# Kernel tuning notes

Measured on AMD Instinct MI355X. Metric: run time of the kernel, lower is better.

Reference implementation:

```python
import jax, jax.numpy as jnp
import numpy as np

EMBED, HEADS, LEVELS, POINTS, CAMS, ZANCH = 256, 8, 4, 8, 6, 4
HEAD_DIM = EMBED // HEADS
NQ, BS = 10000, 1
SHAPES = np.array([[92, 160], [46, 80], [23, 40], [12, 20]], dtype=np.int64)
NV = int((SHAPES[:, 0] * SHAPES[:, 1]).sum())  # 19560


def setup_inputs() -> dict:
    key = jax.random.key(0)
    ks = jax.random.split(key, 10)
    f = lambda k, s, sc=1.0: jax.random.normal(k, s, dtype=jnp.float32) * sc
    lsi = np.concatenate([[0], np.cumsum(SHAPES[:, 0] * SHAPES[:, 1])[:-1]]).astype(np.int64)
    return dict(
        query=f(ks[0], (BS, NQ, EMBED)),
        query_pos=f(ks[1], (BS, NQ, EMBED)),
        value=f(ks[2], (CAMS, NV, BS, EMBED)),
        reference_points=jax.random.uniform(ks[3], (CAMS, BS, NQ, ZANCH, 2), dtype=jnp.float32),
        bev_mask=jax.random.bernoulli(ks[4], 0.3, (CAMS, BS, NQ, ZANCH)),
        spatial_shapes=jnp.asarray(SHAPES),
        level_start_index=jnp.asarray(lsi),
        Wv=f(ks[5], (EMBED, EMBED), 0.02), bv=jnp.zeros((EMBED,), jnp.float32),
        Woff=f(ks[6], (EMBED, HEADS * LEVELS * POINTS * 2), 0.02),
        boff=f(ks[7], (HEADS * LEVELS * POINTS * 2,), 0.5),
        Watt=f(ks[8], (EMBED, HEADS * LEVELS * POINTS), 0.02),
        batt=jnp.zeros((HEADS * LEVELS * POINTS,), jnp.float32),
        Wout=f(ks[9], (EMBED, EMBED), 0.02), bout=jnp.zeros((EMBED,), jnp.float32),
    )


def _bilinear_gather(v2, x, y, H, W):
    # v2: (BH, H*W, hd); x, y: (BH, N) pixel coords. grid_sample bilinear,
    # align_corners=False, padding_mode='zeros' semantics.
    x0 = jnp.floor(x); y0 = jnp.floor(y)
    lx = x - x0; ly = y - y0
    x0i = x0.astype(jnp.int32); y0i = y0.astype(jnp.int32)
    out = jnp.zeros(x.shape + (v2.shape[-1],), v2.dtype)
    for dx, dy, w in ((0, 0, (1 - lx) * (1 - ly)), (1, 0, lx * (1 - ly)),
                      (0, 1, (1 - lx) * ly), (1, 1, lx * ly)):
        xi = x0i + dx; yi = y0i + dy
        valid = (xi >= 0) & (xi < W) & (yi >= 0) & (yi < H)
        idx = jnp.clip(yi, 0, H - 1) * W + jnp.clip(xi, 0, W - 1)
        g = jnp.take_along_axis(v2, idx[..., None], axis=1)
        out = out + g * (w * valid.astype(v2.dtype))[..., None]
    return out


def _ms_deform_attn(q, v, ref, shapes, lsi, Wv, bv, Woff, boff, Watt, batt):
    # q: (B, nq, C); v: (B, nv, C); ref: (B, nq, D, 2)
    B, nq, C = q.shape
    v = (v @ Wv + bv).reshape(B, -1, HEADS, HEAD_DIM)
    off = (q @ Woff + boff).reshape(B, nq, HEADS, LEVELS, POINTS, 2)
    attw = jax.nn.softmax((q @ Watt + batt).reshape(B, nq, HEADS, LEVELS * POINTS), axis=-1)
    attw = attw.reshape(B, nq, HEADS, LEVELS, POINTS)
    # offset normalizer: (w_l, h_l) per level
    norm = jnp.asarray(np.stack([shapes[:, 1], shapes[:, 0]], -1), q.dtype)  # (L, 2)
    off = off / norm[None, None, None, :, None, :]
    off = off.reshape(B, nq, HEADS, LEVELS, POINTS // ZANCH, ZANCH, 2)
    loc = (ref[:, :, None, None, None] + off).reshape(B, nq, HEADS, LEVELS, POINTS, 2)
    acc = jnp.zeros((B, HEADS, nq, HEAD_DIM), q.dtype)
    for l in range(LEVELS):
        H, W = int(shapes[l, 0]), int(shapes[l, 1])
        s = int(lsi[l])
        vl = v[:, s:s + H * W].transpose(0, 2, 1, 3).reshape(B * HEADS, H * W, HEAD_DIM)
        ll = loc[:, :, :, l].transpose(0, 2, 1, 3, 4).reshape(B * HEADS, nq * POINTS, 2)
        x = ll[..., 0] * W - 0.5
        y = ll[..., 1] * H - 0.5
        samp = _bilinear_gather(vl, x, y, H, W).reshape(B, HEADS, nq, POINTS, HEAD_DIM)
        w = attw[:, :, :, l].transpose(0, 2, 1, 3)  # (B, HEADS, nq, POINTS)
        acc = acc + (samp * w[..., None]).sum(3)
    return acc.transpose(0, 2, 1, 3).reshape(B, nq, C)


def reference(query, query_pos, value, reference_points, bev_mask, spatial_shapes,
              level_start_index, Wv, bv, Woff, boff, Watt, batt, Wout, bout):
    shapes = np.asarray(spatial_shapes)
    lsi = np.asarray(level_start_index)
    B, nq, C = query.shape
    cams = value.shape[0]
    q = query + query_pos
    # replicate queries per camera (equivalent to rebatch-by-mask: unselected
    # outputs are masked out before accumulation)
    q_cam = jnp.broadcast_to(q[:, None], (B, cams, nq, C)).reshape(B * cams, nq, C)
    v = value.transpose(2, 0, 1, 3).reshape(B * cams, -1, C)
    ref = reference_points.transpose(1, 0, 2, 3, 4).reshape(B * cams, nq, ZANCH, 2)
    out = _ms_deform_attn(q_cam, v, ref, shapes, lsi, Wv, bv, Woff, boff, Watt, batt)
    out = out.reshape(B, cams, nq, C)
    # query selection per camera uses batch 0 of bev_mask, as in the original
    m = (bev_mask[:, 0].sum(-1) > 0)  # (cams, nq)
    slots = (out * m[None, :, :, None].astype(out.dtype)).sum(1)  # (B, nq, C)
    count = (bev_mask.sum(-1) > 0).astype(query.dtype).transpose(1, 2, 0).sum(-1)
    count = jnp.maximum(count, 1.0)  # (B, nq)
    slots = slots / count[..., None]
    # dropout in eval mode is identity
    return slots @ Wout + bout + query
```

## Files before the change

### kernel.cpp

```cpp
#include <hip/hip_runtime.h>
#include <hip/hip_bf16.h>

constexpr int NQ = 10000, NV = 19560, CAMS = 6, EMBED = 256, HEADS = 8,
              HEAD_DIM = 32, LEVELS = 4, POINTS = 8;
constexpr int MQ_PAD = 10112;
constexpr int MV_PAD = 117376;
constexpr int NBUCK = CAMS * 128;
constexpr int MAXITEMS = CAMS * NQ * 4;

typedef unsigned int u32;
typedef unsigned short u16;
typedef unsigned char u8;
typedef __attribute__((ext_vector_type(8))) short short8v;
typedef __attribute__((ext_vector_type(4))) float f32x4;
typedef __attribute__((ext_vector_type(2))) float f32x2;

__device__ inline u16 f2bf(float f) {
  __hip_bfloat16 b = __float2bfloat16(f);
  return *(u16*)&b;
}
__device__ inline float bf2f(u16 v) { union { u32 i; float f; } x; x.i = (u32)v << 16; return x.f; }

__global__ void conv_bf16_kernel(const float* __restrict__ a, const float* __restrict__ b,
                                 u16* __restrict__ dst, int M, int Mpad) {
  int i = blockIdx.x * blockDim.x + threadIdx.x;
  if (i >= Mpad * 32) return;
  int row = i >> 5;
  int col = (i & 31) * 8;
  u16 o[8];
  if (row < M) {
    const float* pa = a + (size_t)row * 256 + col;
#pragma unroll
    for (int j = 0; j < 8; ++j) {
      float v = pa[j];
      if (b) v += b[(size_t)row * 256 + col + j];
      o[j] = f2bf(v);
    }
  } else {
#pragma unroll
    for (int j = 0; j < 8; ++j) o[j] = 0;
  }
  *(short8v*)&dst[(size_t)row * 256 + col] = *(short8v*)o;
}

__global__ void transpose_w_kernel(const float* __restrict__ src, u16* __restrict__ dst, int N) {
  int g = blockIdx.x * blockDim.x + threadIdx.x;
  if (g >= N * 256) return;
  int n = g >> 8, k = g & 255;
  dst[(size_t)n * 256 + k] = f2bf(src[(size_t)k * N + n]);
}

__device__ inline int orig_off_col(int j) {
  int z = (j >> 7) & 3, h = (j >> 4) & 7, l = (j >> 2) & 3, pi = (j >> 1) & 1, xy = j & 1;
  return h * 64 + l * 16 + (z + 4 * pi) * 2 + xy;
}
__device__ inline int orig_att_col(int j) {
  int z = (j >> 6) & 3, h = (j >> 3) & 7, l = (j >> 1) & 3, pi = j & 1;
  return h * 32 + l * 8 + (z + 4 * pi);
}
__global__ void transpose_wq_kernel(const float* __restrict__ Woff, const float* __restrict__ Watt,
                                    const float* __restrict__ boff, const float* __restrict__ batt,
                                    u16* __restrict__ WqT, float* __restrict__ catb) {
  int g = blockIdx.x * blockDim.x + threadIdx.x;
  if (g >= 768 * 256) return;
  int j = g >> 8, k = g & 255;
  float v;
  if (j < 512) v = Woff[(size_t)k * 512 + orig_off_col(j)];
  else         v = Watt[(size_t)k * 256 + orig_att_col(j - 512)];
  WqT[(size_t)j * 256 + k] = f2bf(v);
  if (k == 0) catb[j] = (j < 512) ? boff[orig_off_col(j)] : batt[orig_att_col(j - 512)];
}

__device__ inline int buck_key(int c, float rx, float ry) {
  int tx = min(max((int)(rx * 16.f), 0), 15);
  int ty = min(max((int)(ry * 8.f), 0), 7);
  return c * 128 + ty * 16 + tx;
}

__global__ void mask_kernel(const int* __restrict__ bev, const float* __restrict__ ref,
                            unsigned char* __restrict__ m, float* __restrict__ cinv,
                            u32* __restrict__ hist) {
  int q = blockIdx.x * blockDim.x + threadIdx.x;
  if (q >= NQ) return;
  int cnt = 0;
  for (int c = 0; c < CAMS; ++c) {
    int any = 0;
    for (int z = 0; z < 4; ++z) any |= bev[((size_t)c * NQ + q) * 4 + z];
    m[c * NQ + q] = (unsigned char)(any != 0);
    cnt += (any != 0);
    if (any) {
      const float* rc = ref + ((size_t)c * NQ + q) * 8;
#pragma unroll
      for (int z = 0; z < 4; ++z)
        atomicAdd(&hist[buck_key(c, rc[z * 2], rc[z * 2 + 1])], 1u);
    }
  }
  cinv[q] = 1.0f / (float)(cnt > 0 ? cnt : 1);
}

__global__ void scan_kernel(const u32* __restrict__ hist, u32* __restrict__ cursor,
                            u32* __restrict__ total) {
  __shared__ u32 tmp[NBUCK];
  int t = threadIdx.x;
  u32 v = hist[t];
  tmp[t] = v;
  __syncthreads();
  for (int d = 1; d < NBUCK; d <<= 1) {
    u32 add = (t >= d) ? tmp[t - d] : 0;
    __syncthreads();
    tmp[t] += add;
    __syncthreads();
  }
  cursor[t] = tmp[t] - v;
  if (t == NBUCK - 1) *total = tmp[t];
}

__global__ void scatter_kernel(const float* __restrict__ ref, const unsigned char* __restrict__ m,
                               u32* __restrict__ cursor, u32* __restrict__ perm) {
  int q = blockIdx.x * blockDim.x + threadIdx.x;
  if (q >= NQ) return;
  for (int c = 0; c < CAMS; ++c) {
    if (!m[c * NQ + q]) continue;
    const float* rc = ref + ((size_t)c * NQ + q) * 8;
#pragma unroll
    for (int z = 0; z < 4; ++z) {
      u32 pos = atomicAdd(&cursor[buck_key(c, rc[z * 2], rc[z * 2 + 1])], 1u);
      perm[pos] = ((u32)c << 16) | ((u32)z << 14) | (u32)q;
    }
  }
}

__global__ __launch_bounds__(256) void gemm_mfma(
    const u16* __restrict__ A, const u16* __restrict__ Bt,
    const float* __restrict__ bias, const float* __restrict__ add,
    void* __restrict__ Cout, void* __restrict__ Cout2, int M, int N, int mode) {
  constexpr int K = 256, BK = 64;
  __shared__ u16 As[128 * BK];
  __shared__ u16 Bs[128 * BK];
  const int tid = threadIdx.x;
  const int lane = tid & 63, w = tid >> 6;
  const int wr = w >> 1, wc = w & 1;
  const int row0 = blockIdx.y * 128, col0 = blockIdx.x * 128;
  f32x4 acc[4][4] = {};

  for (int k0 = 0; k0 < K; k0 += BK) {
    short8v areg[4], breg[4];
#pragma unroll
    for (int j = 0; j < 4; ++j) {
      int e = tid + j * 256;
      int r = e >> 3, cb = (e & 7) * 16;
      areg[j] = *(const short8v*)((const char*)A + ((size_t)(row0 + r) * K + k0) * 2 + cb);
      breg[j] = *(const short8v*)((const char*)Bt + ((size_t)(col0 + r) * K + k0) * 2 + cb);
    }
    __syncthreads();
#pragma unroll
    for (int j = 0; j < 4; ++j) {
      int e = tid + j * 256;
      int r = e >> 3, cb = (e & 7) * 16;
      int sw = cb ^ ((r & 7) << 4);
      *(short8v*)((char*)As + r * 128 + sw) = areg[j];
      *(short8v*)((char*)Bs + r * 128 + sw) = breg[j];
    }
    __syncthreads();
#pragma unroll
    for (int kk = 0; kk < 2; ++kk) {
      short8v af[4], bf[4];
#pragma unroll
      for (int m = 0; m < 4; ++m) {
        int r = wr * 64 + m * 16 + (lane & 15);
        int cb = kk * 64 + (lane >> 4) * 16;
        af[m] = *(const short8v*)((const char*)As + r * 128 + (cb ^ ((r & 7) << 4)));
      }
#pragma unroll
      for (int n = 0; n < 4; ++n) {
        int r = wc * 64 + n * 16 + (lane & 15);
        int cb = kk * 64 + (lane >> 4) * 16;
        bf[n] = *(const short8v*)((const char*)Bs + r * 128 + (cb ^ ((r & 7) << 4)));
      }
#pragma unroll
      for (int m = 0; m < 4; ++m)
#pragma unroll
        for (int n = 0; n < 4; ++n)
          acc[m][n] = __builtin_amdgcn_mfma_f32_16x16x32_bf16(af[m], bf[n], acc[m][n], 0, 0, 0);
    }
  }

#pragma unroll
  for (int m = 0; m < 4; ++m) {
    int rowb = row0 + wr * 64 + m * 16 + (lane >> 4) * 4;
#pragma unroll
    for (int r = 0; r < 4; ++r) {
      int rr = rowb + r;
      if (rr >= M) continue;
#pragma unroll
      for (int n = 0; n < 4; ++n) {
        int col = col0 + wc * 64 + n * 16 + (lane & 15);
        float v = acc[m][n][r] + bias[col];
        if (mode == 0) {
          ((float*)Cout)[(size_t)rr * N + col] = v;
        } else if (mode == 2) {
          ((float*)Cout)[(size_t)rr * N + col] = v + add[(size_t)rr * N + col];
        } else {
          if (col < 512) ((float*)Cout)[(size_t)rr * 512 + col] = v;
          else           ((float*)Cout2)[(size_t)rr * 256 + (col - 512)] = v;
        }
      }
    }
  }
}

__global__ __launch_bounds__(256) void gemm_wv_f32(
    const float* __restrict__ A, const u16* __restrict__ Bt,
    const float* __restrict__ bias, u8* __restrict__ Cout, int M) {
  constexpr int K = 256, BK = 64, N = 256;
  __shared__ u16 As[128 * BK];
  __shared__ u16 Bs[128 * BK];
  const int tid = threadIdx.x;
  const int lane = tid & 63, w = tid >> 6;
  const int wr = w >> 1, wc = w & 1;
  const int row0 = blockIdx.y * 128, col0 = blockIdx.x * 128;
  f32x4 acc[4][4] = {};

  for (int k0 = 0; k0 < K; k0 += BK) {
    short8v areg[4], breg[4];
#pragma unroll
    for (int j = 0; j < 4; ++j) {
      int e = tid + j * 256;
      int r = e >> 3, co = (e & 7) * 8;
      u16 tmp[8];
      if (row0 + r < M) {
        const float* src = A + (size_t)(row0 + r) * K + k0 + co;
        float4 f0 = *(const float4*)src;
        float4 f1 = *(const float4*)(src + 4);
        tmp[0] = f2bf(f0.x); tmp[1] = f2bf(f0.y); tmp[2] = f2bf(f0.z); tmp[3] = f2bf(f0.w);
        tmp[4] = f2bf(f1.x); tmp[5] = f2bf(f1.y); tmp[6] = f2bf(f1.z); tmp[7] = f2bf(f1.w);
      } else {
#pragma unroll
        for (int t = 0; t < 8; ++t) tmp[t] = 0;
      }
      areg[j] = *(short8v*)tmp;
      breg[j] = *(const short8v*)((const char*)Bt + ((size_t)(col0 + r) * K + k0) * 2 + co * 2);
    }
    __syncthreads();
#pragma unroll
    for (int j = 0; j < 4; ++j) {
      int e = tid + j * 256;
      int r = e >> 3, cb = (e & 7) * 16;
      int sw = cb ^ ((r & 7) << 4);
      *(short8v*)((char*)As + r * 128 + sw) = areg[j];
      *(short8v*)((char*)Bs + r * 128 + sw) = breg[j];
    }
    __syncthreads();
#pragma unroll
    for (int kk = 0; kk < 2; ++kk) {
      short8v af[4], bf[4];
#pragma unroll
      for (int m = 0; m < 4; ++m) {
        int r = wr * 64 + m * 16 + (lane & 15);
        int cb = kk * 64 + (lane >> 4) * 16;
        af[m] = *(const short8v*)((const char*)As + r * 128 + (cb ^ ((r & 7) << 4)));
      }
#pragma unroll
      for (int n = 0; n < 4; ++n) {
        int r = wc * 64 + n * 16 + (lane & 15);
        int cb = kk * 64 + (lane >> 4) * 16;
        bf[n] = *(const short8v*)((const char*)Bs + r * 128 + (cb ^ ((r & 7) << 4)));
      }
#pragma unroll
      for (int m = 0; m < 4; ++m)
#pragma unroll
        for (int n = 0; n < 4; ++n)
          acc[m][n] = __builtin_amdgcn_mfma_f32_16x16x32_bf16(af[m], bf[n], acc[m][n], 0, 0, 0);
    }
  }

#pragma unroll
  for (int m = 0; m < 4; ++m) {
    int rowb = row0 + wr * 64 + m * 16 + (lane >> 4) * 4;
#pragma unroll
    for (int r = 0; r < 4; ++r) {
      int rr = rowb + r;
      if (rr >= M) continue;
      int cam = rr / NV;
      int px = rr - cam * NV;
#pragma unroll
      for (int n = 0; n < 4; ++n) {
        int col = col0 + wc * 64 + n * 16 + (lane & 15);
        float v = acc[m][n][r] + bias[col];
        int h = col >> 5, d = col & 31;
        int pk = __builtin_amdgcn_cvt_pk_fp8_f32(v, v, 0, false);
        Cout[(((size_t)cam * HEADS + h) * NV + px) * 32 + d] = (u8)(pk & 0xff);
      }
    }
  }
}

__global__ void softmax_kernel(float* __restrict__ att) {
  int r = blockIdx.x * blockDim.x + threadIdx.x;
  if (r >= NQ * HEADS) return;
  int q = r >> 3, h = r & 7;
  float* base = att + (size_t)q * 256 + h * 8;
  float v[32];
  float mx = -1e30f;
  int n = 0;
#pragma unroll
  for (int z = 0; z < 4; ++z)
#pragma unroll
    for (int l = 0; l < 4; ++l)
#pragma unroll
      for (int pi = 0; pi < 2; ++pi) {
        float x = base[z * 64 + l * 2 + pi];
        v[n++] = x;
        mx = fmaxf(mx, x);
      }
  float sm = 0.f;
#pragma unroll
  for (int i = 0; i < 32; ++i) { v[i] = expf(v[i] - mx); sm += v[i]; }
  float inv = 1.0f / sm;
  n = 0;
#pragma unroll
  for (int z = 0; z < 4; ++z)
#pragma unroll
    for (int l = 0; l < 4; ++l)
#pragma unroll
      for (int pi = 0; pi < 2; ++pi)
        base[z * 64 + l * 2 + pi] = v[n++] * inv;
}

__global__ __launch_bounds__(256, 8) void sample_kernel(
    const u8* __restrict__ vproj, const float* __restrict__ offr,
    const float* __restrict__ attw, const float* __restrict__ ref,
    const u32* __restrict__ perm, const u32* __restrict__ total,
    u16* __restrict__ part2) {
  constexpr int Hs[4] = {92, 46, 23, 12};
  constexpr int Ws[4] = {160, 80, 40, 20};
  constexpr int LSI[4] = {0, 14720, 18400, 19320};
  const int idx = blockIdx.x * 4 + (threadIdx.x >> 6);
  if (idx >= (int)*total) return;
  const u32 item = perm[idx];
  const int c = item >> 16;
  const int z = (item >> 14) & 3;
  const int q = item & 0x3fff;
  const int lane = threadIdx.x & 63;
  const int h = lane >> 3;
  const int pp = (lane >> 2) & 1;
  const int d0 = (lane & 3) * 8;

  const float* rc = ref + ((size_t)c * NQ + q) * 8 + z * 2;
  const float rx = rc[0], ry = rc[1];
  const float* offq = offr + (size_t)q * 512 + z * 128 + h * 16;
  const float* attq = attw + (size_t)q * 256 + z * 64 + h * 8;
  const u8* vch = vproj + ((size_t)c * HEADS + h) * NV * 32 + d0;

  float acc[8] = {};
#pragma unroll 2
  for (int l = 0; l < LEVELS; ++l) {
    const int W = Ws[l], H = Hs[l];
    const u8* vl = vch + (size_t)LSI[l] * 32;
    float2 o = *(const float2*)&offq[l * 4 + pp * 2];
    float a = attq[l * 2 + pp];
    float x = rx * (float)W + o.x - 0.5f;
    float y = ry * (float)H + o.y - 0.5f;
    float x0f = floorf(x), y0f = floorf(y);
    float lx = x - x0f, ly = y - y0f;
    int x0 = (int)x0f, y0 = (int)y0f;
    float fx0 = (x0 >= 0 && x0 < W) ? 1.f : 0.f;
    float fx1 = (x0 >= -1 && x0 < W - 1) ? 1.f : 0.f;
    float fy0 = (y0 >= 0 && y0 < H) ? 1.f : 0.f;
    float fy1 = (y0 >= -1 && y0 < H - 1) ? 1.f : 0.f;
    int x0c = min(max(x0, 0), W - 1);
    int x1c = min(max(x0 + 1, 0), W - 1);
    int y0c = min(max(y0, 0), H - 1);
    int y1c = min(max(y0 + 1, 0), H - 1);
    uint2 v00 = *(const uint2*)(vl + (size_t)(y0c * W + x0c) * 32);
    uint2 v01 = *(const uint2*)(vl + (size_t)(y0c * W + x1c) * 32);
    uint2 v10 = *(const uint2*)(vl + (size_t)(y1c * W + x0c) * 32);
    uint2 v11 = *(const uint2*)(vl + (size_t)(y1c * W + x1c) * 32);
    float c00 = a * (1.f - lx) * (1.f - ly) * fx0 * fy0;
    float c01 = a * lx * (1.f - ly) * fx1 * fy0;
    float c10 = a * (1.f - lx) * ly * fx0 * fy1;
    float c11 = a * lx * ly * fx1 * fy1;
#pragma unroll
    for (int half = 0; half < 2; ++half) {
      u32 w00 = half ? v00.y : v00.x, w01 = half ? v01.y : v01.x;
      u32 w10 = half ? v10.y : v10.x, w11 = half ? v11.y : v11.x;
      f32x2 gA0 = __builtin_amdgcn_cvt_pk_f32_fp8(w00, false);
      f32x2 gA1 = __builtin_amdgcn_cvt_pk_f32_fp8(w00, true);
      f32x2 gB0 = __builtin_amdgcn_cvt_pk_f32_fp8(w01, false);
      f32x2 gB1 = __builtin_amdgcn_cvt_pk_f32_fp8(w01, true);
      f32x2 gC0 = __builtin_amdgcn_cvt_pk_f32_fp8(w10, false);
      f32x2 gC1 = __builtin_amdgcn_cvt_pk_f32_fp8(w10, true);
      f32x2 gD0 = __builtin_amdgcn_cvt_pk_f32_fp8(w11, false);
      f32x2 gD1 = __builtin_amdgcn_cvt_pk_f32_fp8(w11, true);
      int b = half * 4;
      acc[b + 0] += c00 * gA0.x + c01 * gB0.x + c10 * gC0.x + c11 * gD0.x;
      acc[b + 1] += c00 * gA0.y + c01 * gB0.y + c10 * gC0.y + c11 * gD0.y;
      acc[b + 2] += c00 * gA1.x + c01 * gB1.x + c10 * gC1.x + c11 * gD1.x;
      acc[b + 3] += c00 * gA1.y + c01 * gB1.y + c10 * gC1.y + c11 * gD1.y;
    }
  }
#pragma unroll
  for (int d = 0; d < 8; ++d) acc[d] += __shfl_xor(acc[d], 4);
  if (pp == 0) {
    u16 o[8];
#pragma unroll
    for (int d = 0; d < 8; ++d) o[d] = f2bf(acc[d]);
    short8v* sp = (short8v*)&part2[((size_t)(z * CAMS + c) * NQ + q) * EMBED + h * 32 + d0];
    __builtin_nontemporal_store(*(short8v*)o, sp);
  }
}

__global__ void reduce_kernel(const u16* __restrict__ part2, const unsigned char* __restrict__ m,
                              const float* __restrict__ cinv, u16* __restrict__ sbf) {
  int i = blockIdx.x * blockDim.x + threadIdx.x;
  if (i >= MQ_PAD * 32) return;
  int row = i >> 5;
  int col = (i & 31) * 8;
  u16 o[8];
  if (row < NQ) {
    float s[8] = {};
    for (int c = 0; c < CAMS; ++c) {
      if (!m[c * NQ + row]) continue;
#pragma unroll
      for (int z = 0; z < 4; ++z) {
        const short8v* pp = (const short8v*)&part2[((size_t)(z * CAMS + c) * NQ + row) * EMBED + col];
        short8v v = __builtin_nontemporal_load(pp);
#pragma unroll
        for (int j = 0; j < 8; ++j) s[j] += bf2f((u16)v[j]);
      }
    }
    float sc = cinv[row];
#pragma unroll
    for (int j = 0; j < 8; ++j) o[j] = f2bf(s[j] * sc);
  } else {
#pragma unroll
    for (int j = 0; j < 8; ++j) o[j] = 0;
  }
  *(short8v*)&sbf[(size_t)row * 256 + col] = *(short8v*)o;
}

extern "C" void kernel_launch(void* const* d_in, const int* in_sizes, int n_in,
                              void* d_out, int out_size, void* d_ws, size_t ws_size,
                              hipStream_t stream) {
  const float* query     = (const float*)d_in[0];
  const float* query_pos = (const float*)d_in[1];
  const float* value     = (const float*)d_in[2];
  const float* refpts    = (const float*)d_in[3];
  const int*   bev       = (const int*)d_in[4];
  const float* Wv   = (const float*)d_in[7];
  const float* bv   = (const float*)d_in[8];
  const float* Woff = (const float*)d_in[9];
  const float* boff = (const float*)d_in[10];
  const float* Watt = (const float*)d_in[11];
  const float* batt = (const float*)d_in[12];
  const float* Wout = (const float*)d_in[13];
  const float* bout = (const float*)d_in[14];
  float* out = (float*)d_out;

  char* ws = (char*)d_ws;
  auto alloc = [&](size_t bytes) {
    char* p = ws;
    ws += (bytes + 255) & ~(size_t)255;
    return p;
  };
  u16*   qbf   = (u16*)alloc((size_t)MQ_PAD * 256 * 2);
  u16*   sbf   = (u16*)alloc((size_t)MQ_PAD * 256 * 2);
  u16*   WvT   = (u16*)alloc((size_t)256 * 256 * 2);
  u16*   WqT   = (u16*)alloc((size_t)768 * 256 * 2);
  u16*   WoutT = (u16*)alloc((size_t)256 * 256 * 2);
  float* catb  = (float*)alloc((size_t)768 * 4);
  float* offr  = (float*)alloc((size_t)MQ_PAD * 512 * 4);
  float* attw  = (float*)alloc((size_t)MQ_PAD * 256 * 4);
  u8*    vproj = (u8*)alloc((size_t)CAMS * NV * EMBED);
  u16*   part2 = (u16*)alloc((size_t)4 * CAMS * NQ * EMBED * 2);
  float* cinv  = (float*)alloc((size_t)NQ * 4);
  unsigned char* msk = (unsigned char*)alloc((size_t)CAMS * NQ);
  u32*   hist  = (u32*)alloc((size_t)NBUCK * 4);
  u32*   cursor= (u32*)alloc((size_t)NBUCK * 4);
  u32*   total = (u32*)alloc(256);
  u32*   perm  = (u32*)alloc((size_t)MAXITEMS * 4);

  hipMemsetAsync(hist, 0, NBUCK * 4, stream);

  conv_bf16_kernel<<<(MQ_PAD * 32 + 255) / 256, 256, 0, stream>>>(query, query_pos, qbf, NQ, MQ_PAD);
  mask_kernel<<<(NQ + 255) / 256, 256, 0, stream>>>(bev, refpts, msk, cinv, hist);
  transpose_wq_kernel<<<(768 * 256 + 255) / 256, 256, 0, stream>>>(Woff, Watt, boff, batt, WqT, catb);
  transpose_w_kernel<<<256, 256, 0, stream>>>(Wv, WvT, 256);
  transpose_w_kernel<<<256, 256, 0, stream>>>(Wout, WoutT, 256);

  scan_kernel<<<1, NBUCK, 0, stream>>>(hist, cursor, total);
  scatter_kernel<<<(NQ + 255) / 256, 256, 0, stream>>>(refpts, msk, cursor, perm);

  dim3 gQ(768 / 128, MQ_PAD / 128);
  gemm_mfma<<<gQ, 256, 0, stream>>>(qbf, WqT, catb, nullptr, offr, attw, NQ, 768, 3);
  softmax_kernel<<<(NQ * HEADS + 255) / 256, 256, 0, stream>>>(attw);

  dim3 gV(256 / 128, MV_PAD / 128);
  gemm_wv_f32<<<gV, 256, 0, stream>>>(value, WvT, bv, vproj, CAMS * NV);

  sample_kernel<<<MAXITEMS / 4, 256, 0, stream>>>(vproj, offr, attw, refpts, perm, total, part2);

  reduce_kernel<<<(MQ_PAD * 32 + 255) / 256, 256, 0, stream>>>(part2, msk, cinv, sbf);
  dim3 gOut(256 / 128, MQ_PAD / 128);
  gemm_mfma<<<gOut, 256, 0, stream>>>(sbf, WoutT, bout, query, out, nullptr, NQ, 256, 2);
}
```

Before: 456.7 us.

## Widen value-projection GEMM tile to full N and pack sample accumulators

The value-projection GEMM now uses 512-thread blocks with a 128x256 tile covering all output columns. Each fp32 A row is therefore loaded and converted to bf16 once rather than twice, and the grid drops to one dimension. The sampling kernel also accumulates into float2 vectors so the compiler can emit packed FMA instructions. The cost is more LDS per block (B tile doubled) and larger blocks, which may lower occupancy.

```diff
diff --git a/kernel.cpp b/kernel.cpp
--- a/kernel.cpp
+++ b/kernel.cpp
@@ -209,23 +209,23 @@
   }
 }
 
-__global__ __launch_bounds__(256) void gemm_wv_f32(
+__global__ __launch_bounds__(512) void gemm_wv_f32(
     const float* __restrict__ A, const u16* __restrict__ Bt,
     const float* __restrict__ bias, u8* __restrict__ Cout, int M) {
-  constexpr int K = 256, BK = 64, N = 256;
+  constexpr int K = 256, BK = 64;
   __shared__ u16 As[128 * BK];
-  __shared__ u16 Bs[128 * BK];
+  __shared__ u16 Bs[256 * BK];
   const int tid = threadIdx.x;
   const int lane = tid & 63, w = tid >> 6;
-  const int wr = w >> 1, wc = w & 1;
-  const int row0 = blockIdx.y * 128, col0 = blockIdx.x * 128;
+  const int wr = w >> 2, wc = w & 3;
+  const int row0 = blockIdx.x * 128;
   f32x4 acc[4][4] = {};
 
   for (int k0 = 0; k0 < K; k0 += BK) {
-    short8v areg[4], breg[4];
-#pragma unroll
-    for (int j = 0; j < 4; ++j) {
-      int e = tid + j * 256;
+    short8v areg[2], breg[4];
+#pragma unroll
+    for (int j = 0; j < 2; ++j) {
+      int e = tid + j * 512;
       int r = e >> 3, co = (e & 7) * 8;
       u16 tmp[8];
       if (row0 + r < M) {
@@ -239,16 +239,25 @@
         for (int t = 0; t < 8; ++t) tmp[t] = 0;
       }
       areg[j] = *(short8v*)tmp;
-      breg[j] = *(const short8v*)((const char*)Bt + ((size_t)(col0 + r) * K + k0) * 2 + co * 2);
+    }
+#pragma unroll
+    for (int j = 0; j < 4; ++j) {
+      int e = tid + j * 512;
+      int r = e >> 3, cb = (e & 7) * 16;
+      breg[j] = *(const short8v*)((const char*)Bt + ((size_t)r * K + k0) * 2 + cb);
     }
     __syncthreads();
 #pragma unroll
+    for (int j = 0; j < 2; ++j) {
+      int e = tid + j * 512;
+      int r = e >> 3, cb = (e & 7) * 16;
+      *(short8v*)((char*)As + r * 128 + (cb ^ ((r & 7) << 4))) = areg[j];
+    }
+#pragma unroll
     for (int j = 0; j < 4; ++j) {
-      int e = tid + j * 256;
+      int e = tid + j * 512;
       int r = e >> 3, cb = (e & 7) * 16;
-      int sw = cb ^ ((r & 7) << 4);
-      *(short8v*)((char*)As + r * 128 + sw) = areg[j];
-      *(short8v*)((char*)Bs + r * 128 + sw) = breg[j];
+      *(short8v*)((char*)Bs + r * 128 + (cb ^ ((r & 7) << 4))) = breg[j];
     }
     __syncthreads();
 #pragma unroll
@@ -285,7 +294,7 @@
       int px = rr - cam * NV;
 #pragma unroll
       for (int n = 0; n < 4; ++n) {
-        int col = col0 + wc * 64 + n * 16 + (lane & 15);
+        int col = wc * 64 + n * 16 + (lane & 15);
         float v = acc[m][n][r] + bias[col];
         int h = col >> 5, d = col & 31;
         int pk = __builtin_amdgcn_cvt_pk_fp8_f32(v, v, 0, false);
@@ -352,7 +361,7 @@
   const float* attq = attw + (size_t)q * 256 + z * 64 + h * 8;
   const u8* vch = vproj + ((size_t)c * HEADS + h) * NV * 32 + d0;
 
-  float acc[8] = {};
+  f32x2 acc2[4] = {};
 #pragma unroll 2
   for (int l = 0; l < LEVELS; ++l) {
     const int W = Ws[l], H = Hs[l];
@@ -392,19 +401,19 @@
       f32x2 gC1 = __builtin_amdgcn_cvt_pk_f32_fp8(w10, true);
       f32x2 gD0 = __builtin_amdgcn_cvt_pk_f32_fp8(w11, false);
       f32x2 gD1 = __builtin_amdgcn_cvt_pk_f32_fp8(w11, true);
-      int b = half * 4;
-      acc[b + 0] += c00 * gA0.x + c01 * gB0.x + c10 * gC0.x + c11 * gD0.x;
-      acc[b + 1] += c00 * gA0.y + c01 * gB0.y + c10 * gC0.y + c11 * gD0.y;
-      acc[b + 2] += c00 * gA1.x + c01 * gB1.x + c10 * gC1.x + c11 * gD1.x;
-      acc[b + 3] += c00 * gA1.y + c01 * gB1.y + c10 * gC1.y + c11 * gD1.y;
-    }
-  }
-#pragma unroll
-  for (int d = 0; d < 8; ++d) acc[d] += __shfl_xor(acc[d], 4);
+      int b = half * 2;
+      acc2[b + 0] += gA0 * c00 + gB0 * c01 + gC0 * c10 + gD0 * c11;
+      acc2[b + 1] += gA1 * c00 + gB1 * c01 + gC1 * c10 + gD1 * c11;
+    }
+  }
+  float accs[8] = {acc2[0].x, acc2[0].y, acc2[1].x, acc2[1].y,
+                   acc2[2].x, acc2[2].y, acc2[3].x, acc2[3].y};
+#pragma unroll
+  for (int d = 0; d < 8; ++d) accs[d] += __shfl_xor(accs[d], 4);
   if (pp == 0) {
     u16 o[8];
 #pragma unroll
-    for (int d = 0; d < 8; ++d) o[d] = f2bf(acc[d]);
+    for (int d = 0; d < 8; ++d) o[d] = f2bf(accs[d]);
     short8v* sp = (short8v*)&part2[((size_t)(z * CAMS + c) * NQ + q) * EMBED + h * 32 + d0];
     __builtin_nontemporal_store(*(short8v*)o, sp);
   }
@@ -495,8 +504,7 @@
   gemm_mfma<<<gQ, 256, 0, stream>>>(qbf, WqT, catb, nullptr, offr, attw, NQ, 768, 3);
   softmax_kernel<<<(NQ * HEADS + 255) / 256, 256, 0, stream>>>(attw);
 
-  dim3 gV(256 / 128, MV_PAD / 128);
-  gemm_wv_f32<<<gV, 256, 0, stream>>>(value, WvT, bv, vproj, CAMS * NV);
+  gemm_wv_f32<<<MV_PAD / 128, 512, 0, stream>>>(value, WvT, bv, vproj, CAMS * NV);
 
   sample_kernel<<<MAXITEMS / 4, 256, 0, stream>>>(vproj, offr, attw, refpts, perm, total, part2);
 
```

Measured after the change: 443.9 us. -2.8%, faster.
